# Performance work log

Measured on AMD Instinct MI355X. Metric: run time of the kernel, lower is better.

The kernel has to match this reference:

```python
import jax, jax.numpy as jnp
import numpy as np

B = 65536
NQ = 8
NL = 3
FEAT = 64 * 3 * 3 + NQ  # 584


def _conv(x, w, b):
    # x: (B,C,H,W), w: (O,I,3,3), padding=1 -> SAME
    y = jax.lax.conv_general_dilated(
        x, w, window_strides=(1, 1), padding='SAME',
        dimension_numbers=('NCHW', 'OIHW', 'NCHW'))
    return y + b[None, :, None, None]


def _maxpool2(x):
    return jax.lax.reduce_window(
        x, -jnp.inf, jax.lax.max, (1, 1, 2, 2), (1, 1, 2, 2), 'VALID')


def _quantum_sim(x, qp):
    # x: (B,NQ); qp: (NL,NQ,3). Within a layer, qubit q depends only on its own
    # previous state (tanh term), so vectorize over qubits and scan over layers.
    x_next = jnp.roll(x, -1, axis=1)  # x[:, (q+1) % NQ]

    def step(q_state, rot):  # rot: (NQ,3)
        new = jnp.sin(rot[:, 0] * x) * jnp.cos(rot[:, 1] * x_next) \
              + jnp.tanh(rot[:, 2] * q_state)
        return new, None

    q0 = jnp.zeros_like(x)
    qf, _ = jax.lax.scan(step, q0, qp)
    return qf


def setup_inputs() -> dict:
    key = jax.random.key(0)
    ks = jax.random.split(key, 16)

    def w(k, shape, fan_in):
        lim = 1.0 / np.sqrt(fan_in)
        return jax.random.uniform(k, shape, jnp.float32, -lim, lim)

    return {
        'board_state': jax.random.normal(ks[0], (B, 3, 6, 6), jnp.float32),
        'target_positions': jax.random.randint(ks[1], (4, 2), 0, 6).astype(jnp.int64),
        'conv1_w': w(ks[2], (16, 3, 3, 3), 3 * 9), 'conv1_b': w(ks[3], (16,), 3 * 9),
        'conv2_w': w(ks[4], (32, 16, 3, 3), 16 * 9), 'conv2_b': w(ks[5], (32,), 16 * 9),
        'conv3_w': w(ks[6], (64, 32, 3, 3), 32 * 9), 'conv3_b': w(ks[7], (64,), 32 * 9),
        'quantum_params': jax.random.normal(ks[8], (NL, NQ, 3), jnp.float32),
        'pt_w1': w(ks[9], (FEAT, 128), FEAT), 'pt_b1': w(ks[9], (128,), FEAT),
        'pt_w2': w(ks[10], (128, 64), 128), 'pt_b2': w(ks[10], (64,), 128),
        'pt_w3': w(ks[11], (64, 2), 64), 'pt_b3': w(ks[11], (2,), 64),
        'cf_w1': w(ks[12], (FEAT, 64), FEAT), 'cf_b1': w(ks[12], (64,), FEAT),
        'cf_w2': w(ks[13], (64, 1), 64), 'cf_b2': w(ks[13], (1,), 64),
    }


def reference(board_state, target_positions,
              conv1_w, conv1_b, conv2_w, conv2_b, conv3_w, conv3_b,
              quantum_params,
              pt_w1, pt_b1, pt_w2, pt_b2, pt_w3, pt_b3,
              cf_w1, cf_b1, cf_w2, cf_b2):
    b = board_state.shape[0]
    h = jax.nn.relu(_conv(board_state, conv1_w, conv1_b))   # (B,16,6,6)
    h = jax.nn.relu(_conv(h, conv2_w, conv2_b))             # (B,32,6,6)
    h = _maxpool2(h)                                        # (B,32,3,3)
    h = jax.nn.relu(_conv(h, conv3_w, conv3_b))             # (B,64,3,3)
    conv_flat = h.reshape(b, -1)                            # (B,576)

    board_flat = board_state.reshape(b, -1)
    q_feat = _quantum_sim(board_flat[:, :NQ], quantum_params)  # (B,NQ)

    feats = jnp.concatenate([conv_flat, q_feat], axis=1)    # (B,584)

    # piece-type head (Dropout is identity in eval)
    t = jax.nn.relu(feats @ pt_w1 + pt_b1)
    t = jax.nn.relu(t @ pt_w2 + pt_b2)
    type_logits = t @ pt_w3 + pt_b3
    type_probs = jax.nn.softmax(type_logits, axis=1)        # (B,2)

    # confidence head
    c = jax.nn.relu(feats @ cf_w1 + cf_b1)
    confidence = jax.nn.sigmoid(c @ cf_w2 + cf_b2)          # (B,1)

    # target_positions never affect the math (pos_encoding unused in torch source);
    # the same probs/confidence are reported for every position.
    return jnp.concatenate([type_probs, confidence], axis=1)  # (B,3)
```

## Files before the change

kernel.cpp:

```cpp
#include <hip/hip_runtime.h>

typedef _Float16 h8 __attribute__((ext_vector_type(8)));
typedef _Float16 h4 __attribute__((ext_vector_type(4)));
typedef float f32x4 __attribute__((ext_vector_type(4)));
typedef float f32x16 __attribute__((ext_vector_type(16)));

union HU { _Float16 h; unsigned short u; };
__device__ __forceinline__ unsigned short f2h(float f) { HU x; x.h = (_Float16)f; return x.u; }
__device__ __forceinline__ float h2f(unsigned short u) { HU x; x.u = u; return (float)x.h; }

#define MFMA16(a, b, c) __builtin_amdgcn_mfma_f32_16x16x32_f16((a), (b), (c), 0, 0, 0)
#define MFMA32(a, b, c) __builtin_amdgcn_mfma_f32_32x32x16_f16((a), (b), (c), 0, 0, 0)

__global__ void k_prep(const float* __restrict__ w1, const float* __restrict__ w2,
                       const float* __restrict__ w3,
                       const float* __restrict__ ptw1, const float* __restrict__ cfw1,
                       const float* __restrict__ ptw2, const float* __restrict__ ptw3,
                       const float* __restrict__ cfw2,
                       unsigned short* __restrict__ w1f,
                       unsigned short* __restrict__ w2f,
                       unsigned short* __restrict__ w3f,
                       unsigned short* __restrict__ w1hd,
                       unsigned short* __restrict__ w2hd,
                       unsigned short* __restrict__ w3hd) {
    int gid = blockIdx.x * 256 + threadIdx.x;
    int gs = gridDim.x * 256;
    for (int e = gid; e < 1024; e += gs) {
        int f = e >> 9, lane = (e >> 3) & 63, j = e & 7;
        int k = ((lane >> 4) << 3) + j, oc = lane & 15;
        int r, within;
        if (f == 0) { r = k >> 4; within = k & 15; }
        else        { r = 2;      within = k; }
        int tx = within >> 2, ch = within & 3;
        float v = 0.f;
        if (tx < 3 && ch < 3) v = w1[oc * 27 + ch * 9 + r * 3 + tx];
        w1f[e] = f2h(v);
    }
    for (int e = gid; e < 4608; e += gs) {
        int j = e & 7, lane = (e >> 3) & 63, t = e >> 9;
        int oc = lane & 31, k = ((lane >> 5) << 3) + j;
        w2f[e] = f2h(w2[oc * 144 + k * 9 + t]);
    }
    for (int e = gid; e < 18432; e += gs) {
        int j = e & 7, lane = (e >> 3) & 63, fo = e >> 9;
        int oti = fo & 1, t = (fo >> 1) % 9, otp = (fo >> 1) / 9;
        int ic = ((lane >> 4) * 8) + j, oc = (otp * 2 + oti) * 16 + (lane & 15);
        w3f[e] = f2h(w3[oc * 288 + ic * 9 + t]);
    }
    for (int s = gid; s < 608 * 192; s += gs) {
        int k = s / 192, n = s - k * 192;
        float v = 0.f;
        if (k < 584) {
            int f = (k < 576) ? ((k & 63) * 9 + (k >> 6)) : k;
            v = (n < 128) ? ptw1[f * 128 + n] : cfw1[f * 64 + (n - 128)];
        }
        int kk = k >> 5, hi = (k & 31) >> 3, j = k & 7, nt = n >> 4;
        int e = (((kk * 12 + nt) << 6) | (hi << 4) | (n & 15)) << 3 | j;
        w1hd[e] = f2h(v);
    }
    for (int s = gid; s < 8192; s += gs) {
        int k = s >> 6, n = s & 63;
        float v = ptw2[k * 64 + n];
        int kk = k >> 5, hi = (k & 31) >> 3, j = k & 7, nt = n >> 4;
        int e = ((((kk << 2) | nt) << 6) | (hi << 4) | (n & 15)) << 3 | j;
        w2hd[e] = f2h(v);
    }
    for (int e = gid; e < 2048; e += gs) {
        int j = e & 7, lane = (e >> 3) & 63, kk = e >> 9;
        int k = kk * 32 + ((lane >> 4) * 8) + j, n = lane & 15;
        float v = 0.f;
        if (k < 64) { if (n < 2) v = ptw3[k * 2 + n]; }
        else        { if (n == 2) v = cfw2[k - 64]; }
        w3hd[e] = f2h(v);
    }
}

#define BDS4 260
#define BDH4 (16 * BDS4)
#define A1S 584
#define A2S 296
#define FTS 616
#define HSH 200
#define RA_OFF 19712
#define O_OFF 26112
#define LDSTOT 26368

__device__ __forceinline__ f32x16 conv2_pool(const unsigned short* __restrict__ Ab,
                                             const h8 (&W2r)[9], int kh, float b2v,
                                             int pr, int pc) {
    f32x16 pool;
    #pragma unroll
    for (int r = 0; r < 16; r++) pool[r] = 0.f;
    #pragma unroll
    for (int sy = 0; sy < 2; sy++)
        #pragma unroll
        for (int sx = 0; sx < 2; sx++) {
            const int oy = pr * 2 + sy, ox = pc * 2 + sx;
            f32x16 acc;
            #pragma unroll
            for (int r = 0; r < 16; r++) acc[r] = 0.f;
            #pragma unroll
            for (int dy = -1; dy <= 1; dy++) {
                const int ry = oy + dy;
                if (ry < 0 || ry > 5) continue;
                #pragma unroll
                for (int dx = -1; dx <= 1; dx++) {
                    const int rx = ox + dx;
                    if (rx < 0 || rx > 5) continue;
                    h8 a = *(const h8*)&Ab[(ry * 6 + rx) * 16 + kh * 8];
                    acc = MFMA32(a, W2r[(dy + 1) * 3 + (dx + 1)], acc);
                }
            }
            #pragma unroll
            for (int r = 0; r < 16; r++)
                pool[r] = fmaxf(pool[r], acc[r] + b2v);
        }
    return pool;
}

__global__ __launch_bounds__(512, 4) void k_fused(
    const float* __restrict__ board,
    const float* __restrict__ b1, const float* __restrict__ b2,
    const float* __restrict__ b3, const float* __restrict__ qp,
    const unsigned short* __restrict__ w1f,
    const unsigned short* __restrict__ w2f,
    const unsigned short* __restrict__ w3f,
    const unsigned short* __restrict__ w1hd,
    const unsigned short* __restrict__ w2hd,
    const unsigned short* __restrict__ w3hd,
    const float* __restrict__ ptb1, const float* __restrict__ ptb2,
    const float* __restrict__ ptb3, const float* __restrict__ cfb1,
    const float* __restrict__ cfb2,
    float* __restrict__ out)
{
    __shared__ __align__(16) unsigned short LDSH[LDSTOT];
    const int tid = threadIdx.x, wid = tid >> 6, lane = tid & 63;
    const int col = lane & 15, q = lane >> 4;
    const long long gg0 = (long long)blockIdx.x * 32;
    const f32x4 ZERO4 = {0.f, 0.f, 0.f, 0.f};

    unsigned short* Hb = LDSH + RA_OFF;
    float* O = (float*)(LDSH + O_OFF);

    for (int e = tid; e < BDH4 / 4; e += 512)
        ((unsigned long long*)(LDSH + RA_OFF))[e] = 0ULL;
    __syncthreads();

    float qv[2];
    h8 w1r0 = ((const h8*)w1f)[lane];
    h8 w1r1 = ((const h8*)w1f)[64 + lane];
    float b1v = b1[col];
    #pragma unroll
    for (int gi = 0; gi < 2; gi++) {
        for (int e = tid; e < 16 * 108; e += 512) {
            int r2 = e % 108, ch = r2 / 36, p = r2 % 36;
            int ss = e / 108;
            float v = board[(gg0 + gi * 16) * 108 + e];
            LDSH[RA_OFF + ss * BDS4 + ((p / 6 + 1) * 8 + (p % 6) + 1) * 4 + ch] =
                f2h(v);
        }
        __syncthreads();
        if (tid < 128) {
            int ss = tid >> 3, qq = tid & 7;
            int base = RA_OFF + ss * BDS4;
            int p8a = ((qq / 6 + 1) * 8 + (qq % 6) + 1) * 4;
            int e2 = (qq + 1) & 7;
            int p8b = ((e2 / 6 + 1) * 8 + (e2 % 6) + 1) * 4;
            float xq = h2f(LDSH[base + p8a]);
            float xn = h2f(LDSH[base + p8b]);
            float st = 0.f;
            for (int l = 0; l < 3; l++) {
                float a0 = qp[l * 24 + qq * 3], a1 = qp[l * 24 + qq * 3 + 1],
                      a2 = qp[l * 24 + qq * 3 + 2];
                st = sinf(a0 * xq) * cosf(a1 * xn) + tanhf(a2 * st);
            }
            qv[gi] = st;
        }
        {
            unsigned short* A1g = LDSH + gi * 9856;
            const int bs = RA_OFF + col * BDS4;
            const int rsel = q >> 1, wo = (q & 1) * 8;
            const int p0 = wid * 4 + (wid < 4 ? wid : 4);
            const int pe = p0 + (wid < 4 ? 5 : 4);
            for (int p = p0; p < pe; p++) {
                int y = p / 6, x = p % 6;
                int ab1 = bs + ((y + rsel) * 8 + x) * 4 + wo;
                int ab2 = bs + ((y + 2) * 8 + x) * 4 + wo;
                union { h8 v; h4 h[2]; } a1v, a2v;
                a1v.h[0] = *(const h4*)&LDSH[ab1];
                a1v.h[1] = *(const h4*)&LDSH[ab1 + 4];
                a2v.h[0] = *(const h4*)&LDSH[ab2];
                a2v.h[1] = *(const h4*)&LDSH[ab2 + 4];
                f32x4 c = MFMA16(a1v.v, w1r0, ZERO4);
                c = MFMA16(a2v.v, w1r1, c);
                #pragma unroll
                for (int r = 0; r < 4; r++)
                    A1g[(q * 4 + r) * A1S + p * 16 + col] =
                        f2h(fmaxf(c[r] + b1v, 0.f));
            }
        }
        __syncthreads();
    }

    {
        h8 W2r[9];
        #pragma unroll
        for (int t = 0; t < 9; t++)
            W2r[t] = ((const h8*)w2f)[t * 64 + lane];
        const int m32 = lane & 31, kh = lane >> 5;
        const float b2v = b2[m32];
        const unsigned short* Ab = LDSH + (m32 >> 4) * 9856 + (m32 & 15) * A1S;

        if (wid == 0) {
            f32x16 p8 = conv2_pool(Ab, W2r, kh, b2v, 2, 2);
            #pragma unroll
            for (int r = 0; r < 16; r++) {
                int s = (r & 3) + 8 * (r >> 2) + 4 * kh;
                LDSH[RA_OFF + s * 32 + m32] = f2h(p8[r]);
            }
        }
        f32x16 pool = conv2_pool(Ab, W2r, kh, b2v, wid / 3, wid % 3);
        __syncthreads();
        #pragma unroll
        for (int r = 0; r < 16; r++) {
            int s = (r & 3) + 8 * (r >> 2) + 4 * kh;
            LDSH[(s >> 4) * 9856 + (s & 15) * A2S + wid * 32 + m32] = f2h(pool[r]);
        }
        for (int e = tid; e < 1024; e += 512) {
            int s = e >> 5;
            LDSH[(s >> 4) * 9856 + (s & 15) * A2S + 8 * 32 + (e & 31)] =
                LDSH[RA_OFF + e];
        }
    }
    __syncthreads();

    f32x4 c3[9];
    {
        const int g3 = wid >> 2, ot = wid & 3;
        const unsigned short* A2g = LDSH + g3 * 9856;
        h8 W3r[9];
        #pragma unroll
        for (int t = 0; t < 9; t++)
            W3r[t] = ((const h8*)w3f)[((ot >> 1) * 18 + t * 2 + (ot & 1)) * 64 + lane];
        const int sA2 = col * A2S;
        #pragma unroll
        for (int p = 0; p < 9; p++) {
            const int y = p / 3, x = p % 3;
            f32x4 acc = ZERO4;
            #pragma unroll
            for (int t = 0; t < 9; t++) {
                const int sy = y + t / 3 - 1, sx = x + t % 3 - 1;
                if (sy < 0 || sy >= 3 || sx < 0 || sx >= 3) continue;
                h8 a = *(const h8*)&A2g[sA2 + (sy * 3 + sx) * 32 + q * 8];
                acc = MFMA16(a, W3r[t], acc);
            }
            c3[p] = acc;
        }
    }
    __syncthreads();

    {
        const int g3 = wid >> 2, ot = wid & 3;
        float b3v = b3[ot * 16 + col];
        #pragma unroll
        for (int p = 0; p < 9; p++)
            #pragma unroll
            for (int r = 0; r < 4; r++) {
                int row = g3 * 16 + q * 4 + r;
                LDSH[row * FTS + p * 64 + ot * 16 + col] =
                    f2h(fmaxf(c3[p][r] + b3v, 0.f));
            }
        if (tid < 128) {
            int ss = tid >> 3, qq = tid & 7;
            LDSH[ss * FTS + 576 + qq] = f2h(qv[0]);
            LDSH[(ss + 16) * FTS + 576 + qq] = f2h(qv[1]);
        }
        for (int e = tid; e < 1024; e += 512)
            LDSH[(e >> 5) * FTS + 584 + (e & 31)] = 0;
    }
    __syncthreads();

    {
        f32x4 acc[3];
        acc[0] = ZERO4; acc[1] = ZERO4; acc[2] = ZERO4;
        const h8* wp1 = (const h8*)w1hd;
        const int mt = wid & 1, ntb = (wid >> 1) * 3;
        for (int kk = 0; kk < 19; kk++) {
            h8 a = *(const h8*)&LDSH[(mt * 16 + col) * FTS + kk * 32 + q * 8];
            #pragma unroll
            for (int nt = 0; nt < 3; nt++) {
                h8 b = wp1[(kk * 12 + ntb + nt) * 64 + lane];
                acc[nt] = MFMA16(a, b, acc[nt]);
            }
        }
        #pragma unroll
        for (int nt = 0; nt < 3; nt++) {
            int ntg = ntb + nt;
            float bv = (ntg < 8) ? ptb1[ntg * 16 + col] : cfb1[(ntg - 8) * 16 + col];
            #pragma unroll
            for (int r = 0; r < 4; r++)
                Hb[(mt * 16 + q * 4 + r) * HSH + ntg * 16 + col] =
                    f2h(fmaxf(acc[nt][r] + bv, 0.f));
        }
    }
    __syncthreads();

    {
        f32x4 acc2 = ZERO4;
        const h8* wp2 = (const h8*)w2hd;
        const int mt = wid & 1, nt2 = wid >> 1;
        #pragma unroll
        for (int kk = 0; kk < 4; kk++) {
            h8 a = *(const h8*)&Hb[(mt * 16 + col) * HSH + kk * 32 + q * 8];
            h8 b = wp2[(kk * 4 + nt2) * 64 + lane];
            acc2 = MFMA16(a, b, acc2);
        }
        __syncthreads();
        float bv2 = ptb2[nt2 * 16 + col];
        #pragma unroll
        for (int r = 0; r < 4; r++)
            Hb[(mt * 16 + q * 4 + r) * HSH + nt2 * 16 + col] =
                f2h(fmaxf(acc2[r] + bv2, 0.f));
    }
    __syncthreads();

    if (wid < 2) {
        const int mt = wid;
        f32x4 a3 = ZERO4;
        #pragma unroll
        for (int kk = 0; kk < 4; kk++) {
            int base = (kk < 2) ? kk * 32 : kk * 32 + 64;
            h8 a = *(const h8*)&Hb[(mt * 16 + col) * HSH + base + q * 8];
            h8 b = ((const h8*)w3hd)[kk * 64 + lane];
            a3 = MFMA16(a, b, a3);
        }
        if (col < 3) {
            float bv = (col < 2) ? ptb3[col] : cfb2[0];
            #pragma unroll
            for (int r = 0; r < 4; r++)
                O[(mt * 16 + q * 4 + r) * 4 + col] = a3[r] + bv;
        }
        if (lane < 16) {
            int s = mt * 16 + lane;
            float l0 = O[s * 4 + 0], l1 = O[s * 4 + 1], l2 = O[s * 4 + 2];
            float m = fmaxf(l0, l1);
            float e0 = expf(l0 - m), e1 = expf(l1 - m);
            float inv = 1.f / (e0 + e1);
            float* op = out + (gg0 + s) * 3;
            op[0] = e0 * inv;
            op[1] = e1 * inv;
            op[2] = 1.f / (1.f + expf(-l2));
        }
    }
}

extern "C" void kernel_launch(void* const* d_in, const int* in_sizes, int n_in,
                              void* d_out, int out_size, void* d_ws, size_t ws_size,
                              hipStream_t stream) {
    const float* board = (const float*)d_in[0];
    const float* c1w  = (const float*)d_in[2];
    const float* c1b  = (const float*)d_in[3];
    const float* c2w  = (const float*)d_in[4];
    const float* c2b  = (const float*)d_in[5];
    const float* c3w  = (const float*)d_in[6];
    const float* c3b  = (const float*)d_in[7];
    const float* qp   = (const float*)d_in[8];
    const float* ptw1 = (const float*)d_in[9];
    const float* ptb1 = (const float*)d_in[10];
    const float* ptw2 = (const float*)d_in[11];
    const float* ptb2 = (const float*)d_in[12];
    const float* ptw3 = (const float*)d_in[13];
    const float* ptb3 = (const float*)d_in[14];
    const float* cfw1 = (const float*)d_in[15];
    const float* cfb1 = (const float*)d_in[16];
    const float* cfw2 = (const float*)d_in[17];
    const float* cfb2 = (const float*)d_in[18];
    float* out = (float*)d_out;

    int Btot = in_sizes[0] / 108;

    unsigned short* w1f   = (unsigned short*)d_ws;
    unsigned short* w2f   = (unsigned short*)((char*)d_ws + 2048);
    unsigned short* w3f   = (unsigned short*)((char*)d_ws + 20480);
    unsigned short* w1hd  = (unsigned short*)((char*)d_ws + 57344);
    unsigned short* w2hd  = (unsigned short*)((char*)d_ws + 290816);
    unsigned short* w3hd  = (unsigned short*)((char*)d_ws + 307200);

    hipLaunchKernelGGL(k_prep, dim3(256), dim3(256), 0, stream,
                       c1w, c2w, c3w, ptw1, cfw1, ptw2, ptw3, cfw2,
                       w1f, w2f, w3f, w1hd, w2hd, w3hd);
    hipLaunchKernelGGL(k_fused, dim3(Btot / 32), dim3(512), 0, stream,
                       board, c1b, c2b, c3b, qp, w1f, w2f, w3f,
                       w1hd, w2hd, w3hd, ptb1, ptb2, ptb3, cfb1, cfb2, out);
}
```

Measured before the change: 185.2 us.

## Restructure fused CNN kernel to one wavefront per 16-sample block without barriers

The fused kernel moves from 512-thread blocks over 32 samples to single-wave 64-thread blocks over 16 samples. Every stage (conv1, conv2+pool, conv3, MLP heads) now runs in one wavefront, so all __syncthreads barriers go away and LDS use per block drops, which lets more blocks sit on each CU. Conv2 now computes pooled output rows with a zero-pad slot instead of per-wave pool positions, and the board is loaded with vector loads. In exchange, each wave does more serial MFMA work, holds many more weight registers (launch_bounds 64,1), and parallelism inside a block is lost.

```diff
diff --git a/kernel.cpp b/kernel.cpp
--- a/kernel.cpp
+++ b/kernel.cpp
@@ -75,50 +75,17 @@
     }
 }
 
-#define BDS4 260
-#define BDH4 (16 * BDS4)
 #define A1S 584
 #define A2S 296
 #define FTS 616
 #define HSH 200
-#define RA_OFF 19712
-#define O_OFF 26112
-#define LDSTOT 26368
-
-__device__ __forceinline__ f32x16 conv2_pool(const unsigned short* __restrict__ Ab,
-                                             const h8 (&W2r)[9], int kh, float b2v,
-                                             int pr, int pc) {
-    f32x16 pool;
-    #pragma unroll
-    for (int r = 0; r < 16; r++) pool[r] = 0.f;
-    #pragma unroll
-    for (int sy = 0; sy < 2; sy++)
-        #pragma unroll
-        for (int sx = 0; sx < 2; sx++) {
-            const int oy = pr * 2 + sy, ox = pc * 2 + sx;
-            f32x16 acc;
-            #pragma unroll
-            for (int r = 0; r < 16; r++) acc[r] = 0.f;
-            #pragma unroll
-            for (int dy = -1; dy <= 1; dy++) {
-                const int ry = oy + dy;
-                if (ry < 0 || ry > 5) continue;
-                #pragma unroll
-                for (int dx = -1; dx <= 1; dx++) {
-                    const int rx = ox + dx;
-                    if (rx < 0 || rx > 5) continue;
-                    h8 a = *(const h8*)&Ab[(ry * 6 + rx) * 16 + kh * 8];
-                    acc = MFMA32(a, W2r[(dy + 1) * 3 + (dx + 1)], acc);
-                }
-            }
-            #pragma unroll
-            for (int r = 0; r < 16; r++)
-                pool[r] = fmaxf(pool[r], acc[r] + b2v);
-        }
-    return pool;
-}
-
-__global__ __launch_bounds__(512, 4) void k_fused(
+#define BDS4 260
+#define R2H 9856
+#define ZSH 9344
+#define OQH 13056
+#define LDSTOT 14592
+
+__global__ __launch_bounds__(64, 1) void k_fused(
     const float* __restrict__ board,
     const float* __restrict__ b1, const float* __restrict__ b2,
     const float* __restrict__ b3, const float* __restrict__ qp,
@@ -133,220 +100,237 @@
     const float* __restrict__ cfb2,
     float* __restrict__ out)
 {
-    __shared__ __align__(16) unsigned short LDSH[LDSTOT];
-    const int tid = threadIdx.x, wid = tid >> 6, lane = tid & 63;
+    __shared__ __align__(16) unsigned short L[LDSTOT];
+    const int lane = threadIdx.x;
     const int col = lane & 15, q = lane >> 4;
-    const long long gg0 = (long long)blockIdx.x * 32;
+    const long long gg0 = (long long)blockIdx.x * 16;
     const f32x4 ZERO4 = {0.f, 0.f, 0.f, 0.f};
 
-    unsigned short* Hb = LDSH + RA_OFF;
-    float* O = (float*)(LDSH + O_OFF);
-
-    for (int e = tid; e < BDH4 / 4; e += 512)
-        ((unsigned long long*)(LDSH + RA_OFF))[e] = 0ULL;
-    __syncthreads();
-
-    float qv[2];
-    h8 w1r0 = ((const h8*)w1f)[lane];
-    h8 w1r1 = ((const h8*)w1f)[64 + lane];
-    float b1v = b1[col];
-    #pragma unroll
-    for (int gi = 0; gi < 2; gi++) {
-        for (int e = tid; e < 16 * 108; e += 512) {
-            int r2 = e % 108, ch = r2 / 36, p = r2 % 36;
-            int ss = e / 108;
-            float v = board[(gg0 + gi * 16) * 108 + e];
-            LDSH[RA_OFF + ss * BDS4 + ((p / 6 + 1) * 8 + (p % 6) + 1) * 4 + ch] =
-                f2h(v);
-        }
-        __syncthreads();
-        if (tid < 128) {
-            int ss = tid >> 3, qq = tid & 7;
-            int base = RA_OFF + ss * BDS4;
-            int p8a = ((qq / 6 + 1) * 8 + (qq % 6) + 1) * 4;
-            int e2 = (qq + 1) & 7;
-            int p8b = ((e2 / 6 + 1) * 8 + (e2 % 6) + 1) * 4;
-            float xq = h2f(LDSH[base + p8a]);
-            float xn = h2f(LDSH[base + p8b]);
+    for (int e = lane; e < 1040; e += 64)
+        ((unsigned long long*)&L[R2H])[e] = 0ULL;
+    if (lane < 4) ((unsigned long long*)&L[ZSH])[lane] = 0ULL;
+
+    for (int e4 = lane; e4 < 432; e4 += 64) {
+        int ss = e4 / 27, r27 = e4 - ss * 27;
+        const float* bp = board + (gg0 + ss) * 108;
+        f32x4 v = ((const f32x4*)bp)[r27];
+        int f0 = r27 * 4;
+        #pragma unroll
+        for (int j = 0; j < 4; j++) {
+            int f = f0 + j, ch = f / 36, p = f - ch * 36;
+            L[R2H + ss * BDS4 + ((p / 6 + 1) * 8 + (p % 6) + 1) * 4 + ch] =
+                f2h(v[j]);
+        }
+    }
+
+    float qv0 = 0.f, qv1 = 0.f;
+    {
+        int qq = lane & 7, e2 = (qq + 1) & 7;
+        int p8a = ((qq / 6 + 1) * 8 + (qq % 6) + 1) * 4;
+        int p8b = ((e2 / 6 + 1) * 8 + (e2 % 6) + 1) * 4;
+        #pragma unroll
+        for (int i = 0; i < 2; i++) {
+            int base = R2H + (i * 8 + (lane >> 3)) * BDS4;
+            float xq = h2f(L[base + p8a]);
+            float xn = h2f(L[base + p8b]);
             float st = 0.f;
             for (int l = 0; l < 3; l++) {
                 float a0 = qp[l * 24 + qq * 3], a1 = qp[l * 24 + qq * 3 + 1],
                       a2 = qp[l * 24 + qq * 3 + 2];
                 st = sinf(a0 * xq) * cosf(a1 * xn) + tanhf(a2 * st);
             }
-            qv[gi] = st;
-        }
-        {
-            unsigned short* A1g = LDSH + gi * 9856;
-            const int bs = RA_OFF + col * BDS4;
-            const int rsel = q >> 1, wo = (q & 1) * 8;
-            const int p0 = wid * 4 + (wid < 4 ? wid : 4);
-            const int pe = p0 + (wid < 4 ? 5 : 4);
-            for (int p = p0; p < pe; p++) {
-                int y = p / 6, x = p % 6;
-                int ab1 = bs + ((y + rsel) * 8 + x) * 4 + wo;
-                int ab2 = bs + ((y + 2) * 8 + x) * 4 + wo;
-                union { h8 v; h4 h[2]; } a1v, a2v;
-                a1v.h[0] = *(const h4*)&LDSH[ab1];
-                a1v.h[1] = *(const h4*)&LDSH[ab1 + 4];
-                a2v.h[0] = *(const h4*)&LDSH[ab2];
-                a2v.h[1] = *(const h4*)&LDSH[ab2 + 4];
-                f32x4 c = MFMA16(a1v.v, w1r0, ZERO4);
-                c = MFMA16(a2v.v, w1r1, c);
+            if (i == 0) qv0 = st; else qv1 = st;
+        }
+    }
+
+    {
+        h8 w1r0 = ((const h8*)w1f)[lane];
+        h8 w1r1 = ((const h8*)w1f)[64 + lane];
+        float b1v = b1[col];
+        const int bs = R2H + col * BDS4;
+        const int rsel = q >> 1, wo = (q & 1) * 8;
+        for (int p = 0; p < 36; p++) {
+            int y = p / 6, x = p % 6;
+            int ab1 = bs + ((y + rsel) * 8 + x) * 4 + wo;
+            int ab2 = bs + ((y + 2) * 8 + x) * 4 + wo;
+            union { h8 v; h4 h[2]; } a1v, a2v;
+            a1v.h[0] = *(const h4*)&L[ab1];
+            a1v.h[1] = *(const h4*)&L[ab1 + 4];
+            a2v.h[0] = *(const h4*)&L[ab2];
+            a2v.h[1] = *(const h4*)&L[ab2 + 4];
+            f32x4 c = MFMA16(a1v.v, w1r0, ZERO4);
+            c = MFMA16(a2v.v, w1r1, c);
+            #pragma unroll
+            for (int r = 0; r < 4; r++)
+                L[(q * 4 + r) * A1S + p * 16 + col] =
+                    f2h(fmaxf(c[r] + b1v, 0.f));
+        }
+    }
+
+    {
+        h8 W2r[9];
+        #pragma unroll
+        for (int t = 0; t < 9; t++) W2r[t] = ((const h8*)w2f)[t * 64 + lane];
+        const int m32 = lane & 31;
+        const float b2v = b2[m32];
+        const int samp = lane & 15, half = (lane >> 4) & 1, kh = lane >> 5;
+        const int aBase = samp * A1S + kh * 8;
+        const int zoff = ZSH + kh * 8;
+        #pragma unroll
+        for (int pr = 0; pr < 3; pr++) {
+            f32x16 pool[3];
+            #pragma unroll
+            for (int xp = 0; xp < 3; xp++)
                 #pragma unroll
-                for (int r = 0; r < 4; r++)
-                    A1g[(q * 4 + r) * A1S + p * 16 + col] =
-                        f2h(fmaxf(c[r] + b1v, 0.f));
-            }
-        }
-        __syncthreads();
-    }
-
-    {
-        h8 W2r[9];
-        #pragma unroll
-        for (int t = 0; t < 9; t++)
-            W2r[t] = ((const h8*)w2f)[t * 64 + lane];
-        const int m32 = lane & 31, kh = lane >> 5;
-        const float b2v = b2[m32];
-        const unsigned short* Ab = LDSH + (m32 >> 4) * 9856 + (m32 & 15) * A1S;
-
-        if (wid == 0) {
-            f32x16 p8 = conv2_pool(Ab, W2r, kh, b2v, 2, 2);
-            #pragma unroll
-            for (int r = 0; r < 16; r++) {
-                int s = (r & 3) + 8 * (r >> 2) + 4 * kh;
-                LDSH[RA_OFF + s * 32 + m32] = f2h(p8[r]);
-            }
-        }
-        f32x16 pool = conv2_pool(Ab, W2r, kh, b2v, wid / 3, wid % 3);
-        __syncthreads();
-        #pragma unroll
-        for (int r = 0; r < 16; r++) {
-            int s = (r & 3) + 8 * (r >> 2) + 4 * kh;
-            LDSH[(s >> 4) * 9856 + (s & 15) * A2S + wid * 32 + m32] = f2h(pool[r]);
-        }
-        for (int e = tid; e < 1024; e += 512) {
-            int s = e >> 5;
-            LDSH[(s >> 4) * 9856 + (s & 15) * A2S + 8 * 32 + (e & 31)] =
-                LDSH[RA_OFF + e];
-        }
-    }
-    __syncthreads();
-
-    f32x4 c3[9];
-    {
-        const int g3 = wid >> 2, ot = wid & 3;
-        const unsigned short* A2g = LDSH + g3 * 9856;
-        h8 W3r[9];
-        #pragma unroll
-        for (int t = 0; t < 9; t++)
-            W3r[t] = ((const h8*)w3f)[((ot >> 1) * 18 + t * 2 + (ot & 1)) * 64 + lane];
-        const int sA2 = col * A2S;
-        #pragma unroll
+                for (int r = 0; r < 16; r++) pool[xp][r] = 0.f;
+            #pragma unroll
+            for (int yy = 0; yy < 2; yy++) {
+                const int y = pr * 2 + yy;
+                #pragma unroll
+                for (int xp = 0; xp < 3; xp++) {
+                    f32x16 acc;
+                    #pragma unroll
+                    for (int r = 0; r < 16; r++) acc[r] = 0.f;
+                    #pragma unroll
+                    for (int dy = -1; dy <= 1; dy++) {
+                        const int ys = y + dy;
+                        if (ys < 0 || ys > 5) continue;
+                        #pragma unroll
+                        for (int dx = -1; dx <= 1; dx++) {
+                            int aoff = aBase + (ys * 6 + xp * 2 + half + dx) * 16;
+                            if (xp == 0 && dx == -1) aoff = half ? aoff : zoff;
+                            if (xp == 2 && dx == 1)  aoff = half ? zoff : aoff;
+                            h8 a = *(const h8*)&L[aoff];
+                            acc = MFMA32(a, W2r[(dy + 1) * 3 + dx + 1], acc);
+                        }
+                    }
+                    #pragma unroll
+                    for (int r = 0; r < 16; r++)
+                        pool[xp][r] = fmaxf(pool[xp][r], acc[r] + b2v);
+                }
+            }
+            #pragma unroll
+            for (int xp = 0; xp < 3; xp++)
+                #pragma unroll
+                for (int rr = 0; rr < 8; rr++) {
+                    float v = fmaxf(pool[xp][rr], pool[xp][rr + 8]);
+                    int ss = (rr & 3) + 8 * (rr >> 2) + 4 * kh;
+                    L[R2H + ss * A2S + (pr * 3 + xp) * 32 + m32] = f2h(v);
+                }
+        }
+    }
+
+    {
+        h8 w3r[4][9];
+        #pragma unroll
+        for (int t = 0; t < 9; t++) {
+            w3r[0][t] = ((const h8*)w3f)[(t * 2 + 0) * 64 + lane];
+            w3r[1][t] = ((const h8*)w3f)[(t * 2 + 1) * 64 + lane];
+            w3r[2][t] = ((const h8*)w3f)[((9 + t) * 2 + 0) * 64 + lane];
+            w3r[3][t] = ((const h8*)w3f)[((9 + t) * 2 + 1) * 64 + lane];
+        }
+        float b3v0 = b3[col], b3v1 = b3[16 + col];
+        float b3v2 = b3[32 + col], b3v3 = b3[48 + col];
+        const int sA2 = R2H + (lane & 15) * A2S + q * 8;
         for (int p = 0; p < 9; p++) {
-            const int y = p / 3, x = p % 3;
-            f32x4 acc = ZERO4;
+            int y = p / 3, x = p - y * 3;
+            f32x4 a0 = ZERO4, a1 = ZERO4, a2 = ZERO4, a3 = ZERO4;
             #pragma unroll
             for (int t = 0; t < 9; t++) {
-                const int sy = y + t / 3 - 1, sx = x + t % 3 - 1;
-                if (sy < 0 || sy >= 3 || sx < 0 || sx >= 3) continue;
-                h8 a = *(const h8*)&A2g[sA2 + (sy * 3 + sx) * 32 + q * 8];
-                acc = MFMA16(a, W3r[t], acc);
-            }
-            c3[p] = acc;
-        }
-    }
-    __syncthreads();
-
-    {
-        const int g3 = wid >> 2, ot = wid & 3;
-        float b3v = b3[ot * 16 + col];
-        #pragma unroll
-        for (int p = 0; p < 9; p++)
+                int sy = y + t / 3 - 1, sx = x + t % 3 - 1;
+                if ((unsigned)sy < 3u && (unsigned)sx < 3u) {
+                    h8 a = *(const h8*)&L[sA2 + (sy * 3 + sx) * 32];
+                    a0 = MFMA16(a, w3r[0][t], a0);
+                    a1 = MFMA16(a, w3r[1][t], a1);
+                    a2 = MFMA16(a, w3r[2][t], a2);
+                    a3 = MFMA16(a, w3r[3][t], a3);
+                }
+            }
             #pragma unroll
             for (int r = 0; r < 4; r++) {
-                int row = g3 * 16 + q * 4 + r;
-                LDSH[row * FTS + p * 64 + ot * 16 + col] =
-                    f2h(fmaxf(c3[p][r] + b3v, 0.f));
-            }
-        if (tid < 128) {
-            int ss = tid >> 3, qq = tid & 7;
-            LDSH[ss * FTS + 576 + qq] = f2h(qv[0]);
-            LDSH[(ss + 16) * FTS + 576 + qq] = f2h(qv[1]);
-        }
-        for (int e = tid; e < 1024; e += 512)
-            LDSH[(e >> 5) * FTS + 584 + (e & 31)] = 0;
-    }
-    __syncthreads();
-
-    {
-        f32x4 acc[3];
-        acc[0] = ZERO4; acc[1] = ZERO4; acc[2] = ZERO4;
+                int row = (q * 4 + r) * FTS + p * 64 + col;
+                L[row +  0] = f2h(fmaxf(a0[r] + b3v0, 0.f));
+                L[row + 16] = f2h(fmaxf(a1[r] + b3v1, 0.f));
+                L[row + 32] = f2h(fmaxf(a2[r] + b3v2, 0.f));
+                L[row + 48] = f2h(fmaxf(a3[r] + b3v3, 0.f));
+            }
+        }
+        L[(lane >> 3) * FTS + 576 + (lane & 7)] = f2h(qv0);
+        L[((lane >> 3) + 8) * FTS + 576 + (lane & 7)] = f2h(qv1);
+        for (int e = lane; e < 512; e += 64)
+            L[(e >> 5) * FTS + 584 + (e & 31)] = 0;
+    }
+
+    {
+        f32x4 h1[12];
+        #pragma unroll
+        for (int n = 0; n < 12; n++) h1[n] = ZERO4;
         const h8* wp1 = (const h8*)w1hd;
-        const int mt = wid & 1, ntb = (wid >> 1) * 3;
+        const int aFT = (lane & 15) * FTS + q * 8;
         for (int kk = 0; kk < 19; kk++) {
-            h8 a = *(const h8*)&LDSH[(mt * 16 + col) * FTS + kk * 32 + q * 8];
-            #pragma unroll
-            for (int nt = 0; nt < 3; nt++) {
-                h8 b = wp1[(kk * 12 + ntb + nt) * 64 + lane];
-                acc[nt] = MFMA16(a, b, acc[nt]);
-            }
-        }
-        #pragma unroll
-        for (int nt = 0; nt < 3; nt++) {
-            int ntg = ntb + nt;
-            float bv = (ntg < 8) ? ptb1[ntg * 16 + col] : cfb1[(ntg - 8) * 16 + col];
+            h8 a = *(const h8*)&L[aFT + kk * 32];
+            #pragma unroll
+            for (int nt = 0; nt < 12; nt++) {
+                h8 b = wp1[(kk * 12 + nt) * 64 + lane];
+                h1[nt] = MFMA16(a, b, h1[nt]);
+            }
+        }
+        #pragma unroll
+        for (int nt = 0; nt < 12; nt++) {
+            float bv = (nt < 8) ? ptb1[nt * 16 + col] : cfb1[(nt - 8) * 16 + col];
             #pragma unroll
             for (int r = 0; r < 4; r++)
-                Hb[(mt * 16 + q * 4 + r) * HSH + ntg * 16 + col] =
-                    f2h(fmaxf(acc[nt][r] + bv, 0.f));
-        }
-    }
-    __syncthreads();
-
-    {
-        f32x4 acc2 = ZERO4;
-        const h8* wp2 = (const h8*)w2hd;
-        const int mt = wid & 1, nt2 = wid >> 1;
+                L[R2H + (q * 4 + r) * HSH + nt * 16 + col] =
+                    f2h(fmaxf(h1[nt][r] + bv, 0.f));
+        }
+    }
+
+    {
+        f32x4 h2[4];
+        #pragma unroll
+        for (int n = 0; n < 4; n++) h2[n] = ZERO4;
+        const int aHb = R2H + (lane & 15) * HSH + q * 8;
         #pragma unroll
         for (int kk = 0; kk < 4; kk++) {
-            h8 a = *(const h8*)&Hb[(mt * 16 + col) * HSH + kk * 32 + q * 8];
-            h8 b = wp2[(kk * 4 + nt2) * 64 + lane];
-            acc2 = MFMA16(a, b, acc2);
-        }
-        __syncthreads();
-        float bv2 = ptb2[nt2 * 16 + col];
-        #pragma unroll
-        for (int r = 0; r < 4; r++)
-            Hb[(mt * 16 + q * 4 + r) * HSH + nt2 * 16 + col] =
-                f2h(fmaxf(acc2[r] + bv2, 0.f));
-    }
-    __syncthreads();
-
-    if (wid < 2) {
-        const int mt = wid;
+            h8 a = *(const h8*)&L[aHb + kk * 32];
+            #pragma unroll
+            for (int nt = 0; nt < 4; nt++) {
+                h8 b = ((const h8*)w2hd)[(kk * 4 + nt) * 64 + lane];
+                h2[nt] = MFMA16(a, b, h2[nt]);
+            }
+        }
+        #pragma unroll
+        for (int nt = 0; nt < 4; nt++) {
+            float bv2 = ptb2[nt * 16 + col];
+            #pragma unroll
+            for (int r = 0; r < 4; r++)
+                L[R2H + (q * 4 + r) * HSH + nt * 16 + col] =
+                    f2h(fmaxf(h2[nt][r] + bv2, 0.f));
+        }
+    }
+
+    {
         f32x4 a3 = ZERO4;
         #pragma unroll
         for (int kk = 0; kk < 4; kk++) {
             int base = (kk < 2) ? kk * 32 : kk * 32 + 64;
-            h8 a = *(const h8*)&Hb[(mt * 16 + col) * HSH + base + q * 8];
+            h8 a = *(const h8*)&L[R2H + (lane & 15) * HSH + base + q * 8];
             h8 b = ((const h8*)w3hd)[kk * 64 + lane];
             a3 = MFMA16(a, b, a3);
         }
+        float* O = (float*)&L[OQH];
         if (col < 3) {
             float bv = (col < 2) ? ptb3[col] : cfb2[0];
             #pragma unroll
             for (int r = 0; r < 4; r++)
-                O[(mt * 16 + q * 4 + r) * 4 + col] = a3[r] + bv;
+                O[(q * 4 + r) * 4 + col] = a3[r] + bv;
         }
         if (lane < 16) {
-            int s = mt * 16 + lane;
-            float l0 = O[s * 4 + 0], l1 = O[s * 4 + 1], l2 = O[s * 4 + 2];
+            float l0 = O[lane * 4 + 0], l1 = O[lane * 4 + 1], l2 = O[lane * 4 + 2];
             float m = fmaxf(l0, l1);
             float e0 = expf(l0 - m), e1 = expf(l1 - m);
             float inv = 1.f / (e0 + e1);
-            float* op = out + (gg0 + s) * 3;
+            float* op = out + (gg0 + lane) * 3;
             op[0] = e0 * inv;
             op[1] = e1 * inv;
             op[2] = 1.f / (1.f + expf(-l2));
@@ -389,7 +373,7 @@
     hipLaunchKernelGGL(k_prep, dim3(256), dim3(256), 0, stream,
                        c1w, c2w, c3w, ptw1, cfw1, ptw2, ptw3, cfw2,
                        w1f, w2f, w3f, w1hd, w2hd, w3hd);
-    hipLaunchKernelGGL(k_fused, dim3(Btot / 32), dim3(512), 0, stream,
+    hipLaunchKernelGGL(k_fused, dim3(Btot / 16), dim3(64), 0, stream,
                        board, c1b, c2b, c3b, qp, w1f, w2f, w3f,
                        w1hd, w2hd, w3hd, ptb1, ptb2, ptb3, cfb1, cfb2, out);
 }
```

Result: slower. 316.7 us (+71.0%).
